# Performance work log

Hardware: AMD Instinct MI355X
Metric: run time of the kernel (lower is better)

The kernel has to match this reference:

```python
import jax, jax.numpy as jnp
from jax import lax
import numpy as np

L, B, D = 2048, 8, 1024
LN_EPS = 1e-5


def setup_inputs() -> dict:
    key = jax.random.key(0)
    k1, k2 = jax.random.split(key)
    x = jax.random.normal(k1, (L, B, D), dtype=jnp.float32)
    c0 = jnp.zeros((B, D), dtype=jnp.float32)
    # nn.Linear(D, 3D, bias=False): weight shape (3D, D), y = x @ W.T
    W = jax.random.normal(k2, (3 * D, D), dtype=jnp.float32) * (1.0 / np.sqrt(D))
    ln_w = jnp.ones((D,), dtype=jnp.float32)
    ln_b = jnp.zeros((D,), dtype=jnp.float32)
    return {"x": x, "c0": c0, "W": W, "ln_w": ln_w, "ln_b": ln_b}


def reference(x, c0, W, ln_w, ln_b):
    # ufr = x @ W.T : (L,B,3D)
    ufr = jnp.einsum('lbd,ed->lbe', x, W)
    u, f, r = jnp.split(ufr, 3, axis=-1)
    f = jax.nn.sigmoid(f)
    r = jax.nn.sigmoid(r)

    # sequential SRU recurrence: c_t = f_t * c_{t-1} + (1 - f_t) * u_t
    def step(c, fu):
        f_t, u_t = fu
        c = f_t * c + (1.0 - f_t) * u_t
        return c, c

    last_c, c_stack = lax.scan(step, c0, (f, u))  # c_stack: (L,B,D)

    hs = r * jnp.tanh(c_stack) + (1.0 - r) * x
    g = jax.nn.gelu(hs, approximate=False)  # torch F.gelu default = exact erf

    mu = jnp.mean(g, axis=-1, keepdims=True)
    var = jnp.mean(jnp.square(g - mu), axis=-1, keepdims=True)
    out = (g - mu) * lax.rsqrt(var + LN_EPS) * ln_w + ln_b
    return (out, last_c)
```

## Files before the change

### kernel.cpp

```cpp
#include <hip/hip_runtime.h>

typedef unsigned short u16;
typedef unsigned int   u32;
typedef __attribute__((ext_vector_type(8))) __bf16 bf16x8;
typedef __attribute__((ext_vector_type(4))) float  f32x4;

#define L_SEQ  2048
#define BATCH  8
#define DIM    1024
#define ROWS   16384
#define N3     3072
#define NCHUNK 128
#define LCHUNK 16
#define NCHAIN 8192

struct __align__(8) us4 { u16 x, y, z, w; };

__device__ __forceinline__ float b2f(u16 h) {
  return __builtin_bit_cast(float, (u32)h << 16);
}
__device__ __forceinline__ u32 pk2(float a, float b) {
  u32 r;
  asm("v_cvt_pk_bf16_f32 %0, %1, %2" : "=v"(r) : "v"(a), "v"(b));
  return r;
}
__device__ __forceinline__ u16 f2b(float f) {
  u32 u = __builtin_bit_cast(u32, f);
  return (u16)((u + 0x7fffu + ((u >> 16) & 1u)) >> 16);
}
__device__ __forceinline__ f32x4 mf(bf16x8 a, bf16x8 b, f32x4 c) {
  return __builtin_amdgcn_mfma_f32_16x16x32_bf16(a, b, c, 0, 0, 0);
}

__global__ void k_pack(const float* __restrict__ x, const float* __restrict__ W,
                       u16* __restrict__ apk, u16* __restrict__ wpk) {
  const int NA = 128 * 32 * 8 * 64;
  const int NB = 12 * 32 * 16 * 64;
  int i = blockIdx.x * 256 + threadIdx.x;
  const int stride = gridDim.x * 256;
  for (; i < NA + NB; i += stride) {
    const float* src; u16* dst;
    if (i < NA) {
      int lane = i & 63, fg = (i >> 6) & 7, t = (i >> 9) & 31, mt = i >> 14;
      int row = mt * 128 + fg * 16 + (lane & 15);
      int k   = t * 32 + (lane >> 4) * 8;
      src = x + (size_t)row * DIM + k;
      dst = apk + (size_t)i * 8;
    } else {
      int j = i - NA;
      int lane = j & 63, c = (j >> 6) & 15, t = (j >> 10) & 31, nt = j >> 15;
      int col = nt * 256 + c * 16 + (lane & 15);
      int k   = t * 32 + (lane >> 4) * 8;
      src = W + (size_t)col * DIM + k;
      dst = wpk + (size_t)j * 8;
    }
    float4 v0 = *(const float4*)src;
    float4 v1 = *(const float4*)(src + 4);
    uint4 o;
    o.x = pk2(v0.x, v0.y); o.y = pk2(v0.z, v0.w);
    o.z = pk2(v1.x, v1.y); o.w = pk2(v1.z, v1.w);
    *(uint4*)dst = o;
  }
}

__device__ __forceinline__ void gl_lds16(const u16* g, u16* l) {
  __builtin_amdgcn_global_load_lds((const __attribute__((address_space(1))) void*)g,
                                   (__attribute__((address_space(3))) void*)l,
                                   16, 0, 0);
}

__global__ __launch_bounds__(512, 4) void k_gemm_v6(const u16* __restrict__ apk,
                                                    const u16* __restrict__ wpk,
                                                    u16* __restrict__ C) {
  __shared__ u16 lds[12288];
  const int tid  = threadIdx.x;
  const int lane = tid & 63;
  const int wid  = tid >> 6;
  const int wm = wid >> 2, wn = wid & 3;
  const int lr = lane & 15, lk = lane >> 4;

  const int bid = blockIdx.x;
  const int xcd = bid & 7;
  const int r   = bid >> 3;
  const int byl = r / 12;
  const int bx  = r - byl * 12;
  const int by  = xcd * 16 + byl;

  const u16* srcA = apk + ((((size_t)by * 32) * 8 + wid) * 64 + lane) * 8;
  const u16* srcB = wpk + ((((size_t)bx * 32) * 16 + wn * 4) * 64 + lane) * 8;

  u16* d0 = &lds[wid * 512 + lane * 8];
  u16* d1 = d0 + 4096;
  u16* d2 = d0 + 8192;
  const u16* ldsA = &lds[wm * 2048 + lane * 8];

  f32x4 acc[4][4] = {};
  bf16x8 A0, A1, A2, A3, B0, B1, B2, B3;

  {
    const u16* gb = srcB;
    A0 = *(const bf16x8*)(gb);
    A1 = *(const bf16x8*)(gb + 512);
    A2 = *(const bf16x8*)(gb + 1024);
    A3 = *(const bf16x8*)(gb + 1536);
  }
  __builtin_amdgcn_sched_barrier(0);
  gl_lds16(srcA, d0);
  gl_lds16(srcA + 4096, d1);
  asm volatile("s_waitcnt vmcnt(1)" ::: "memory");
  asm volatile("s_barrier" ::: "memory");

#define GBODY(T, RB, DN, U0,U1,U2,U3, L0,L1,L2,L3, LOADB, STAGEA, LASTP) {   \
    if (STAGEA) gl_lds16(srcA + (size_t)((T) + 2) * 4096, DN);               \
    __builtin_amdgcn_sched_barrier(0);                                       \
    if (LOADB) {                                                             \
      const u16* gb_ = srcB + (size_t)((T) + 1) * 8192;                      \
      L0 = *(const bf16x8*)(gb_);                                            \
      L1 = *(const bf16x8*)(gb_ + 512);                                      \
      L2 = *(const bf16x8*)(gb_ + 1024);                                     \
      L3 = *(const bf16x8*)(gb_ + 1536);                                     \
    }                                                                        \
    __builtin_amdgcn_sched_barrier(0);                                       \
    const u16* rb_ = ldsA + (RB) * 4096;                                     \
    bf16x8 av0 = *(const bf16x8*)(rb_);                                      \
    bf16x8 av1 = *(const bf16x8*)(rb_ + 512);                                \
    bf16x8 av2 = *(const bf16x8*)(rb_ + 1024);                               \
    bf16x8 av3 = *(const bf16x8*)(rb_ + 1536);                               \
    __builtin_amdgcn_s_setprio(1);                                           \
    acc[0][0]=mf(av0,U0,acc[0][0]); acc[0][1]=mf(av0,U1,acc[0][1]);          \
    acc[0][2]=mf(av0,U2,acc[0][2]); acc[0][3]=mf(av0,U3,acc[0][3]);          \
    acc[1][0]=mf(av1,U0,acc[1][0]); acc[1][1]=mf(av1,U1,acc[1][1]);          \
    acc[1][2]=mf(av1,U2,acc[1][2]); acc[1][3]=mf(av1,U3,acc[1][3]);          \
    acc[2][0]=mf(av2,U0,acc[2][0]); acc[2][1]=mf(av2,U1,acc[2][1]);          \
    acc[2][2]=mf(av2,U2,acc[2][2]); acc[2][3]=mf(av2,U3,acc[2][3]);          \
    acc[3][0]=mf(av3,U0,acc[3][0]); acc[3][1]=mf(av3,U1,acc[3][1]);          \
    acc[3][2]=mf(av3,U2,acc[3][2]); acc[3][3]=mf(av3,U3,acc[3][3]);          \
    __builtin_amdgcn_s_setprio(0);                                           \
    if (!(LASTP)) asm volatile("s_barrier" ::: "memory");                    \
  }

  for (int t6 = 0; t6 < 30; t6 += 6) {
    GBODY(t6 + 0, 0, d2, A0,A1,A2,A3, B0,B1,B2,B3, 1, 1, 0)
    GBODY(t6 + 1, 1, d0, B0,B1,B2,B3, A0,A1,A2,A3, 1, 1, 0)
    GBODY(t6 + 2, 2, d1, A0,A1,A2,A3, B0,B1,B2,B3, 1, 1, 0)
    GBODY(t6 + 3, 0, d2, B0,B1,B2,B3, A0,A1,A2,A3, 1, 1, 0)
    GBODY(t6 + 4, 1, d0, A0,A1,A2,A3, B0,B1,B2,B3, 1, 1, 0)
    GBODY(t6 + 5, 2, d1, B0,B1,B2,B3, A0,A1,A2,A3, 1, 1, 0)
  }
  GBODY(30, 0, d2, A0,A1,A2,A3, B0,B1,B2,B3, 1, 0, 0)
  GBODY(31, 1, d0, B0,B1,B2,B3, A0,A1,A2,A3, 0, 0, 1)
#undef GBODY

  const bool act = (bx >= 4);
#pragma unroll
  for (int m = 0; m < 4; ++m) {
    const int row0 = by * 128 + wm * 64 + m * 16 + lk * 4;
#pragma unroll
    for (int n = 0; n < 4; ++n) {
      const int col = bx * 256 + wn * 64 + n * 16 + lr;
#pragma unroll
      for (int j = 0; j < 4; ++j) {
        float v = acc[m][n][j];
        if (act) v = 1.f / (1.f + __expf(-v));
        C[(size_t)(row0 + j) * N3 + col] = f2b(v);
      }
    }
  }
}

__global__ __launch_bounds__(256) void k_gemm_reg(const float* __restrict__ A,
                                                  const float* __restrict__ B,
                                                  u16* __restrict__ C) {
  __shared__ u16 lds[8192];
  const int tid  = threadIdx.x;
  const int lane = tid & 63;
  const int wid  = tid >> 6;
  const int wm = wid >> 1, wn = wid & 1;
  const int lr = lane & 15, lk = lane >> 4;
  const int mBase = blockIdx.y << 7;
  const int nBase = blockIdx.x << 7;

  f32x4 acc[4][4] = {};
  const int aoff = (wm * 64 + lr) * 32 + lk * 8;
  const int boff = 4096 + (wn * 64 + lr) * 32 + lk * 8;

  for (int k0 = 0; k0 < DIM; k0 += 32) {
#pragma unroll
    for (int q = 0; q < 4; ++q) {
      const int i  = q * 256 + tid;
      const int rr = i >> 3;
      const int cc = (i & 7) << 2;
      float4 va = *(const float4*)(A + (size_t)(mBase + rr) * DIM + k0 + cc);
      float4 vb = *(const float4*)(B + (size_t)(nBase + rr) * DIM + k0 + cc);
      uint2 pa; pa.x = pk2(va.x, va.y); pa.y = pk2(va.z, va.w);
      uint2 pb; pb.x = pk2(vb.x, vb.y); pb.y = pk2(vb.z, vb.w);
      *(uint2*)&lds[rr * 32 + cc] = pa;
      *(uint2*)&lds[4096 + rr * 32 + cc] = pb;
    }
    __syncthreads();
    bf16x8 av[4], bv[4];
#pragma unroll
    for (int m = 0; m < 4; ++m) av[m] = *(const bf16x8*)&lds[aoff + m * 512];
#pragma unroll
    for (int n = 0; n < 4; ++n) bv[n] = *(const bf16x8*)&lds[boff + n * 512];
#pragma unroll
    for (int m = 0; m < 4; ++m)
#pragma unroll
      for (int n = 0; n < 4; ++n)
        acc[m][n] = mf(av[m], bv[n], acc[m][n]);
    __syncthreads();
  }

  const bool act = (nBase >= DIM);
#pragma unroll
  for (int m = 0; m < 4; ++m) {
    const int row0 = mBase + wm * 64 + m * 16 + lk * 4;
#pragma unroll
    for (int n = 0; n < 4; ++n) {
      const int col = nBase + wn * 64 + n * 16 + lr;
#pragma unroll
      for (int j = 0; j < 4; ++j) {
        float v = acc[m][n][j];
        if (act) v = 1.f / (1.f + __expf(-v));
        C[(size_t)(row0 + j) * N3 + col] = f2b(v);
      }
    }
  }
}

__global__ void k_scanA(const u16* __restrict__ ufr, float* __restrict__ P,
                        float* __restrict__ V) {
  int idx = blockIdx.x * 256 + threadIdx.x;
  int j  = idx >> 11;
  int cg = idx & 2047;
  int b  = cg >> 8;
  int d0 = (cg & 255) << 2;
  const u16* p = ufr + (size_t)((j * LCHUNK) * BATCH + b) * N3 + d0;
  float prod0 = 1.f, prod1 = 1.f, prod2 = 1.f, prod3 = 1.f;
  float v0 = 0.f, v1 = 0.f, v2 = 0.f, v3 = 0.f;
  for (int t = 0; t < LCHUNK; ++t) {
    us4 uu = *(const us4*)(p);
    us4 ff = *(const us4*)(p + DIM);
    float f0 = b2f(ff.x), f1 = b2f(ff.y), f2 = b2f(ff.z), f3 = b2f(ff.w);
    v0 = f0 * v0 + (1.f - f0) * b2f(uu.x); prod0 *= f0;
    v1 = f1 * v1 + (1.f - f1) * b2f(uu.y); prod1 *= f1;
    v2 = f2 * v2 + (1.f - f2) * b2f(uu.z); prod2 *= f2;
    v3 = f3 * v3 + (1.f - f3) * b2f(uu.w); prod3 *= f3;
    p += BATCH * N3;
  }
  const int base = j * NCHAIN + b * DIM + d0;
  *(float4*)&P[base] = make_float4(prod0, prod1, prod2, prod3);
  *(float4*)&V[base] = make_float4(v0, v1, v2, v3);
}

__global__ void k_scanB(const float* __restrict__ c0, const float* __restrict__ P,
                        const float* __restrict__ V, float* __restrict__ S,
                        float* __restrict__ lastc) {
  int chain = blockIdx.x * 256 + threadIdx.x;
  float c = c0[chain];
  for (int j = 0; j < NCHUNK; ++j) {
    S[j * NCHAIN + chain] = c;
    c = P[j * NCHAIN + chain] * c + V[j * NCHAIN + chain];
  }
  lastc[chain] = c;
}

__global__ __launch_bounds__(256) void k_scanln(const u16* __restrict__ ufr,
                                                const float* __restrict__ S,
                                                const float* __restrict__ x,
                                                const float* __restrict__ lnw,
                                                const float* __restrict__ lnb,
                                                float* __restrict__ out) {
  const int j = blockIdx.x >> 3;
  const int b = blockIdx.x & 7;
  const int tid = threadIdx.x;
  const int d0 = tid << 2;
  const int lane = tid & 63, wid = tid >> 6;

  float4 c4  = *(const float4*)&S[j * NCHAIN + b * DIM + d0];
  float c0v = c4.x, c1v = c4.y, c2v = c4.z, c3v = c4.w;
  const float4 wv = *(const float4*)(lnw + d0);
  const float4 bv = *(const float4*)(lnb + d0);

  const u16*   pu = ufr + (size_t)((j * LCHUNK) * BATCH + b) * N3 + d0;
  const float* px = x   + (size_t)((j * LCHUNK) * BATCH + b) * DIM + d0;
  float*       po = out + (size_t)((j * LCHUNK) * BATCH + b) * DIM + d0;

  __shared__ float red1[2][4], red2[2][4];

  us4 cu = *(const us4*)(pu);
  us4 cf = *(const us4*)(pu + DIM);
  us4 cr = *(const us4*)(pu + 2 * DIM);
  float4 cx = *(const float4*)px;

  for (int t = 0; t < LCHUNK; ++t) {
    const size_t advU = (t < LCHUNK - 1) ? (size_t)BATCH * N3 : 0;
    const size_t advX = (t < LCHUNK - 1) ? (size_t)BATCH * DIM : 0;
    us4 nu = *(const us4*)(pu + advU);
    us4 nf = *(const us4*)(pu + advU + DIM);
    us4 nr = *(const us4*)(pu + advU + 2 * DIM);
    float4 nx = *(const float4*)(px + advX);

    float g0, g1, g2, g3;
    {
      float f = b2f(cf.x); c0v = f * c0v + (1.f - f) * b2f(cu.x);
      float rr = b2f(cr.x);
      float hs = rr * tanhf(c0v) + (1.f - rr) * cx.x;
      g0 = 0.5f * hs * (1.f + erff(hs * 0.70710678118654752f));
    }
    {
      float f = b2f(cf.y); c1v = f * c1v + (1.f - f) * b2f(cu.y);
      float rr = b2f(cr.y);
      float hs = rr * tanhf(c1v) + (1.f - rr) * cx.y;
      g1 = 0.5f * hs * (1.f + erff(hs * 0.70710678118654752f));
    }
    {
      float f = b2f(cf.z); c2v = f * c2v + (1.f - f) * b2f(cu.z);
      float rr = b2f(cr.z);
      float hs = rr * tanhf(c2v) + (1.f - rr) * cx.z;
      g2 = 0.5f * hs * (1.f + erff(hs * 0.70710678118654752f));
    }
    {
      float f = b2f(cf.w); c3v = f * c3v + (1.f - f) * b2f(cu.w);
      float rr = b2f(cr.w);
      float hs = rr * tanhf(c3v) + (1.f - rr) * cx.w;
      g3 = 0.5f * hs * (1.f + erff(hs * 0.70710678118654752f));
    }

    float s1 = g0 + g1 + g2 + g3;
    float s2 = g0 * g0 + g1 * g1 + g2 * g2 + g3 * g3;
#pragma unroll
    for (int off = 32; off > 0; off >>= 1) {
      s1 += __shfl_down(s1, off, 64);
      s2 += __shfl_down(s2, off, 64);
    }
    const int pb = t & 1;
    if (lane == 0) { red1[pb][wid] = s1; red2[pb][wid] = s2; }
    __syncthreads();
    float S1 = red1[pb][0] + red1[pb][1] + red1[pb][2] + red1[pb][3];
    float S2 = red2[pb][0] + red2[pb][1] + red2[pb][2] + red2[pb][3];
    float mu  = S1 * (1.f / DIM);
    float var = S2 * (1.f / DIM) - mu * mu;
    float inv = rsqrtf(var + 1e-5f);
    float4 o;
    o.x = (g0 - mu) * inv * wv.x + bv.x;
    o.y = (g1 - mu) * inv * wv.y + bv.y;
    o.z = (g2 - mu) * inv * wv.z + bv.z;
    o.w = (g3 - mu) * inv * wv.w + bv.w;
    *(float4*)po = o;

    cu = nu; cf = nf; cr = nr; cx = nx;
    pu += BATCH * N3;
    px += BATCH * DIM;
    po += BATCH * DIM;
  }
}

extern "C" void kernel_launch(void* const* d_in, const int* in_sizes, int n_in,
                              void* d_out, int out_size, void* d_ws, size_t ws_size,
                              hipStream_t stream) {
  (void)in_sizes; (void)n_in; (void)out_size;
  const float* x   = (const float*)d_in[0];
  const float* c0  = (const float*)d_in[1];
  const float* W   = (const float*)d_in[2];
  const float* lnw = (const float*)d_in[3];
  const float* lnb = (const float*)d_in[4];
  float* out   = (float*)d_out;
  float* lastc = out + (size_t)ROWS * DIM;

  char* ws = (char*)d_ws;

  u16* ufr; float *P, *V, *S;
  const size_t FULL_NEED = 140509184;
  if (ws_size >= FULL_NEED) {
    u16* apk = (u16*)ws;
    u16* wpk = (u16*)(ws + 33554432);
    ufr = (u16*)(ws + 39845888);
    P   = (float*)ws;
    V   = (float*)(ws + 4194304);
    S   = (float*)(ws + 8388608);
    k_pack<<<2048, 256, 0, stream>>>(x, W, apk, wpk);
    k_gemm_v6<<<1536, 512, 0, stream>>>(apk, wpk, ufr);
  } else {
    ufr = (u16*)ws;
    P   = (float*)(ws + 100663296);
    V   = (float*)(ws + 104857600);
    S   = (float*)(ws + 109051904);
    dim3 g1(N3 / 128, ROWS / 128);
    k_gemm_reg<<<g1, 256, 0, stream>>>(x, W, ufr);
  }

  k_scanA<<<1024, 256, 0, stream>>>(ufr, P, V);
  k_scanB<<<NCHAIN / 256, 256, 0, stream>>>(c0, P, V, S, lastc);
  k_scanln<<<NCHUNK * BATCH, 256, 0, stream>>>(ufr, S, x, lnw, lnb, out);
}
```

Before: 190.5 us.

## Enlarge GEMM block tile to 256x256 with LDS-staged A and B

The packed-bf16 GEMM moves from a 128x256 block tile to a 256x256 tile, halving the grid to 768 blocks and doubling per-wave accumulators to 8x4 MFMA tiles. Both A and B are now staged into LDS with double buffering through global_load_lds, where before B was streamed straight into registers. The A packing layout is changed to match 256-row tiles. The aim is more operand reuse per loaded byte and less global traffic for B. The cost is higher register and LDS use, with occupancy dropping from 4 to 2 blocks per CU, and more barriers per k-step.

```diff
diff --git a/kernel.cpp b/kernel.cpp
--- a/kernel.cpp
+++ b/kernel.cpp
@@ -34,15 +34,15 @@
 
 __global__ void k_pack(const float* __restrict__ x, const float* __restrict__ W,
                        u16* __restrict__ apk, u16* __restrict__ wpk) {
-  const int NA = 128 * 32 * 8 * 64;
+  const int NA = 64 * 32 * 16 * 64;
   const int NB = 12 * 32 * 16 * 64;
   int i = blockIdx.x * 256 + threadIdx.x;
   const int stride = gridDim.x * 256;
   for (; i < NA + NB; i += stride) {
     const float* src; u16* dst;
     if (i < NA) {
-      int lane = i & 63, fg = (i >> 6) & 7, t = (i >> 9) & 31, mt = i >> 14;
-      int row = mt * 128 + fg * 16 + (lane & 15);
+      int lane = i & 63, fg = (i >> 6) & 15, t = (i >> 10) & 31, mt = i >> 15;
+      int row = mt * 256 + fg * 16 + (lane & 15);
       int k   = t * 32 + (lane >> 4) * 8;
       src = x + (size_t)row * DIM + k;
       dst = apk + (size_t)i * 8;
@@ -69,10 +69,10 @@
                                    16, 0, 0);
 }
 
-__global__ __launch_bounds__(512, 4) void k_gemm_v6(const u16* __restrict__ apk,
+__global__ __launch_bounds__(512, 2) void k_gemm_v8(const u16* __restrict__ apk,
                                                     const u16* __restrict__ wpk,
                                                     u16* __restrict__ C) {
-  __shared__ u16 lds[12288];
+  __shared__ u16 lds[32768];
   const int tid  = threadIdx.x;
   const int lane = tid & 63;
   const int wid  = tid >> 6;
@@ -84,77 +84,102 @@
   const int r   = bid >> 3;
   const int byl = r / 12;
   const int bx  = r - byl * 12;
-  const int by  = xcd * 16 + byl;
-
-  const u16* srcA = apk + ((((size_t)by * 32) * 8 + wid) * 64 + lane) * 8;
-  const u16* srcB = wpk + ((((size_t)bx * 32) * 16 + wn * 4) * 64 + lane) * 8;
-
-  u16* d0 = &lds[wid * 512 + lane * 8];
-  u16* d1 = d0 + 4096;
-  u16* d2 = d0 + 8192;
-  const u16* ldsA = &lds[wm * 2048 + lane * 8];
-
-  f32x4 acc[4][4] = {};
-  bf16x8 A0, A1, A2, A3, B0, B1, B2, B3;
-
-  {
-    const u16* gb = srcB;
-    A0 = *(const bf16x8*)(gb);
-    A1 = *(const bf16x8*)(gb + 512);
-    A2 = *(const bf16x8*)(gb + 1024);
-    A3 = *(const bf16x8*)(gb + 1536);
-  }
-  __builtin_amdgcn_sched_barrier(0);
-  gl_lds16(srcA, d0);
-  gl_lds16(srcA + 4096, d1);
-  asm volatile("s_waitcnt vmcnt(1)" ::: "memory");
-  asm volatile("s_barrier" ::: "memory");
-
-#define GBODY(T, RB, DN, U0,U1,U2,U3, L0,L1,L2,L3, LOADB, STAGEA, LASTP) {   \
-    if (STAGEA) gl_lds16(srcA + (size_t)((T) + 2) * 4096, DN);               \
-    __builtin_amdgcn_sched_barrier(0);                                       \
-    if (LOADB) {                                                             \
-      const u16* gb_ = srcB + (size_t)((T) + 1) * 8192;                      \
-      L0 = *(const bf16x8*)(gb_);                                            \
-      L1 = *(const bf16x8*)(gb_ + 512);                                      \
-      L2 = *(const bf16x8*)(gb_ + 1024);                                     \
-      L3 = *(const bf16x8*)(gb_ + 1536);                                     \
-    }                                                                        \
-    __builtin_amdgcn_sched_barrier(0);                                       \
-    const u16* rb_ = ldsA + (RB) * 4096;                                     \
-    bf16x8 av0 = *(const bf16x8*)(rb_);                                      \
-    bf16x8 av1 = *(const bf16x8*)(rb_ + 512);                                \
-    bf16x8 av2 = *(const bf16x8*)(rb_ + 1024);                               \
-    bf16x8 av3 = *(const bf16x8*)(rb_ + 1536);                               \
-    __builtin_amdgcn_s_setprio(1);                                           \
-    acc[0][0]=mf(av0,U0,acc[0][0]); acc[0][1]=mf(av0,U1,acc[0][1]);          \
-    acc[0][2]=mf(av0,U2,acc[0][2]); acc[0][3]=mf(av0,U3,acc[0][3]);          \
-    acc[1][0]=mf(av1,U0,acc[1][0]); acc[1][1]=mf(av1,U1,acc[1][1]);          \
-    acc[1][2]=mf(av1,U2,acc[1][2]); acc[1][3]=mf(av1,U3,acc[1][3]);          \
-    acc[2][0]=mf(av2,U0,acc[2][0]); acc[2][1]=mf(av2,U1,acc[2][1]);          \
-    acc[2][2]=mf(av2,U2,acc[2][2]); acc[2][3]=mf(av2,U3,acc[2][3]);          \
-    acc[3][0]=mf(av3,U0,acc[3][0]); acc[3][1]=mf(av3,U1,acc[3][1]);          \
-    acc[3][2]=mf(av3,U2,acc[3][2]); acc[3][3]=mf(av3,U3,acc[3][3]);          \
-    __builtin_amdgcn_s_setprio(0);                                           \
-    if (!(LASTP)) asm volatile("s_barrier" ::: "memory");                    \
-  }
-
-  for (int t6 = 0; t6 < 30; t6 += 6) {
-    GBODY(t6 + 0, 0, d2, A0,A1,A2,A3, B0,B1,B2,B3, 1, 1, 0)
-    GBODY(t6 + 1, 1, d0, B0,B1,B2,B3, A0,A1,A2,A3, 1, 1, 0)
-    GBODY(t6 + 2, 2, d1, A0,A1,A2,A3, B0,B1,B2,B3, 1, 1, 0)
-    GBODY(t6 + 3, 0, d2, B0,B1,B2,B3, A0,A1,A2,A3, 1, 1, 0)
-    GBODY(t6 + 4, 1, d0, A0,A1,A2,A3, B0,B1,B2,B3, 1, 1, 0)
-    GBODY(t6 + 5, 2, d1, B0,B1,B2,B3, A0,A1,A2,A3, 1, 1, 0)
-  }
-  GBODY(30, 0, d2, A0,A1,A2,A3, B0,B1,B2,B3, 1, 0, 0)
-  GBODY(31, 1, d0, B0,B1,B2,B3, A0,A1,A2,A3, 0, 0, 1)
-#undef GBODY
+  const int by  = xcd * 8 + byl;
+
+  const u16* apkA = apk + (((size_t)by * 32 * 16 + wid) * 64 + lane) * 8;
+  const u16* wpkB = wpk + (((size_t)bx * 32 * 16 + wid) * 64 + lane) * 8;
+  u16* ldsT = &lds[wid * 512 + lane * 8];
+
+  const u16* aB = &lds[wm * 4096 + lane * 8];
+  const u16* bB = &lds[16384 + (wn >> 1) * 4096 + (wn & 1) * 2048 + lane * 8];
+
+  f32x4 acc[8][4] = {};
+
+#define STAGE_A(T, SB) { \
+    gl_lds16(apkA + (size_t)(T) * 8192,            ldsT + (SB));          \
+    gl_lds16(apkA + (size_t)(T) * 8192 + 4096,     ldsT + (SB) + 4096); }
+#define STAGE_B(T, SB) { \
+    gl_lds16(wpkB + (size_t)(T) * 8192,            ldsT + 16384 + (SB));          \
+    gl_lds16(wpkB + (size_t)(T) * 8192 + 4096,     ldsT + 16384 + (SB) + 4096); }
+
+#define MFMA16(M4, a0,a1,a2,a3) \
+    acc[(M4)+0][0]=mf(a0,b0,acc[(M4)+0][0]); acc[(M4)+0][1]=mf(a0,b1,acc[(M4)+0][1]); \
+    acc[(M4)+0][2]=mf(a0,b2,acc[(M4)+0][2]); acc[(M4)+0][3]=mf(a0,b3,acc[(M4)+0][3]); \
+    acc[(M4)+1][0]=mf(a1,b0,acc[(M4)+1][0]); acc[(M4)+1][1]=mf(a1,b1,acc[(M4)+1][1]); \
+    acc[(M4)+1][2]=mf(a1,b2,acc[(M4)+1][2]); acc[(M4)+1][3]=mf(a1,b3,acc[(M4)+1][3]); \
+    acc[(M4)+2][0]=mf(a2,b0,acc[(M4)+2][0]); acc[(M4)+2][1]=mf(a2,b1,acc[(M4)+2][1]); \
+    acc[(M4)+2][2]=mf(a2,b2,acc[(M4)+2][2]); acc[(M4)+2][3]=mf(a2,b3,acc[(M4)+2][3]); \
+    acc[(M4)+3][0]=mf(a3,b0,acc[(M4)+3][0]); acc[(M4)+3][1]=mf(a3,b1,acc[(M4)+3][1]); \
+    acc[(M4)+3][2]=mf(a3,b2,acc[(M4)+3][2]); acc[(M4)+3][3]=mf(a3,b3,acc[(M4)+3][3]);
+
+#define PHASE0(RB, STG, VM) { \
+    STG \
+    __builtin_amdgcn_sched_barrier(0); \
+    if ((VM) == 1) asm volatile("s_waitcnt vmcnt(2)" ::: "memory"); \
+    else           asm volatile("s_waitcnt vmcnt(0)" ::: "memory"); \
+    asm volatile("s_barrier" ::: "memory"); \
+    const u16* ab_ = aB + (RB); \
+    bf16x8 a0 = *(const bf16x8*)(ab_); \
+    bf16x8 a1 = *(const bf16x8*)(ab_ + 512); \
+    bf16x8 a2 = *(const bf16x8*)(ab_ + 1024); \
+    bf16x8 a3 = *(const bf16x8*)(ab_ + 1536); \
+    const u16* bb_ = bB + (RB); \
+    bf16x8 b0 = *(const bf16x8*)(bb_); \
+    bf16x8 b1 = *(const bf16x8*)(bb_ + 512); \
+    bf16x8 b2 = *(const bf16x8*)(bb_ + 1024); \
+    bf16x8 b3 = *(const bf16x8*)(bb_ + 1536); \
+    asm volatile("s_waitcnt lgkmcnt(0)" ::: "memory"); \
+    __builtin_amdgcn_sched_barrier(0); \
+    __builtin_amdgcn_s_setprio(1); \
+    MFMA16(0, a0, a1, a2, a3) \
+    __builtin_amdgcn_s_setprio(0); \
+    asm volatile("s_barrier" ::: "memory"); \
+  }
+
+#define PHASEX(RB, STG) { \
+    const u16* ab_ = aB + (RB) + 2048; \
+    bf16x8 a0 = *(const bf16x8*)(ab_); \
+    bf16x8 a1 = *(const bf16x8*)(ab_ + 512); \
+    bf16x8 a2 = *(const bf16x8*)(ab_ + 1024); \
+    bf16x8 a3 = *(const bf16x8*)(ab_ + 1536); \
+    const u16* bb_ = bB + (RB); \
+    bf16x8 b0 = *(const bf16x8*)(bb_); \
+    bf16x8 b1 = *(const bf16x8*)(bb_ + 512); \
+    bf16x8 b2 = *(const bf16x8*)(bb_ + 1024); \
+    bf16x8 b3 = *(const bf16x8*)(bb_ + 1536); \
+    __builtin_amdgcn_sched_barrier(0); \
+    STG \
+    __builtin_amdgcn_sched_barrier(0); \
+    asm volatile("s_barrier" ::: "memory"); \
+    asm volatile("s_waitcnt lgkmcnt(0)" ::: "memory"); \
+    __builtin_amdgcn_sched_barrier(0); \
+    __builtin_amdgcn_s_setprio(1); \
+    MFMA16(4, a0, a1, a2, a3) \
+    __builtin_amdgcn_s_setprio(0); \
+    asm volatile("s_barrier" ::: "memory"); \
+  }
+
+  STAGE_A(0, 0)
+  STAGE_B(0, 0)
+
+  for (int t = 0; t < 31; ++t) {
+    const int RB = (t & 1) * 8192;
+    const int SB = RB ^ 8192;
+    PHASE0(RB, STAGE_A(t + 1, SB), 1)
+    PHASEX(RB, STAGE_B(t + 1, SB))
+  }
+  PHASE0(8192, {}, 0)
+  PHASEX(8192, {})
+#undef PHASE0
+#undef PHASEX
+#undef MFMA16
+#undef STAGE_A
+#undef STAGE_B
 
   const bool act = (bx >= 4);
 #pragma unroll
-  for (int m = 0; m < 4; ++m) {
-    const int row0 = by * 128 + wm * 64 + m * 16 + lk * 4;
+  for (int m = 0; m < 8; ++m) {
+    const int row0 = by * 256 + wm * 128 + m * 16 + lk * 4;
 #pragma unroll
     for (int n = 0; n < 4; ++n) {
       const int col = bx * 256 + wn * 64 + n * 16 + lr;
@@ -380,7 +405,7 @@
     V   = (float*)(ws + 4194304);
     S   = (float*)(ws + 8388608);
     k_pack<<<2048, 256, 0, stream>>>(x, W, apk, wpk);
-    k_gemm_v6<<<1536, 512, 0, stream>>>(apk, wpk, ufr);
+    k_gemm_v8<<<768, 512, 0, stream>>>(apk, wpk, ufr);
   } else {
     ufr = (u16*)ws;
     P   = (float*)(ws + 100663296);
```

Result: slower. 199.3 us (+4.6%).
